# Optimization experiments

Hardware: AMD Instinct MI355X
Metric: run time of the kernel (lower is better)

Reference implementation:

```python
import jax, jax.numpy as jnp
import numpy as np

N_NODES = 100000


def setup_inputs() -> dict:
    key = jax.random.key(0)
    k1, k2, k3, k4 = jax.random.split(key, 4)
    E = 1600000
    D_IN, D_OUT = 128, 128
    feat = jax.random.normal(k1, (N_NODES, D_IN), dtype=jnp.float32)
    src = jax.random.randint(k2, (E,), 0, N_NODES, dtype=jnp.int32)
    dst = jax.random.randint(k3, (E,), 0, N_NODES, dtype=jnp.int32)
    # xavier_uniform for weight [in, out]
    limit = float(np.sqrt(6.0 / (D_IN + D_OUT)))
    weight = jax.random.uniform(k4, (D_IN, D_OUT), dtype=jnp.float32,
                                minval=-limit, maxval=limit)
    bias = jnp.zeros((D_OUT,), dtype=jnp.float32)
    return {"feat": feat, "weight": weight, "bias": bias, "src": src, "dst": dst}


def reference(feat, weight, bias, src, dst):
    # in-degree normalization: norm_i = 1/sqrt(in_deg(i)); clamp deg>=1 to avoid inf
    deg = jax.ops.segment_sum(jnp.ones(src.shape[0], dtype=jnp.float32), dst,
                              num_segments=N_NODES)
    norm = jax.lax.rsqrt(jnp.maximum(deg, 1.0))[:, None]  # [N,1]
    h = feat * norm
    # update_all(copy_src, sum): scatter-sum src features into dst nodes (SpMM)
    agg = jax.ops.segment_sum(h[src], dst, num_segments=N_NODES)  # [N, D_in]
    # in_feats == out_feats -> aggregate first, then dense transform
    rst = agg @ weight          # [N, D_out]
    rst = rst * norm + bias
    return rst
```

## Files before the change

### kernel.cpp

```cpp
#include <hip/hip_runtime.h>


constexpr int N_NODES = 100000;
constexpr int D = 128;
constexpr int NB = 256;
constexpr int GROUP = (N_NODES + NB - 1) / NB;
constexpr int CAP = 14336;
constexpr int CONVB = 1280;
constexpr int RPAD = 136;

typedef float f32x4 __attribute__((ext_vector_type(4)));
typedef short short8 __attribute__((ext_vector_type(8)));
typedef unsigned uint4v __attribute__((ext_vector_type(4)));

__device__ __forceinline__ ushort f2bf(float x) {
    unsigned u = __float_as_uint(x);
    return (ushort)((u + 0x7fffu + ((u >> 16) & 1u)) >> 16);
}
__device__ __forceinline__ float bf2f(ushort h) {
    return __uint_as_float(((unsigned)h) << 16);
}

__global__ __launch_bounds__(256) void p1_histo_conv(const int* __restrict__ dst, int E,
                                                     int* __restrict__ bhist,
                                                     const float* __restrict__ W,
                                                     ushort* __restrict__ whi,
                                                     ushort* __restrict__ wlo,
                                                     const float* __restrict__ feat,
                                                     uint2* __restrict__ ft2) {
    int t = threadIdx.x, blk = blockIdx.x;
    if (blk >= NB) {
        int base = (blk - NB) * 256 + t;
        int stride = CONVB * 256;
        for (int i = base; i < N_NODES * 32; i += stride) {
            f32x4 v = ((const f32x4*)feat)[i];
            uint2 o;
            o.x = (unsigned)f2bf(v[0]) | ((unsigned)f2bf(v[1]) << 16);
            o.y = (unsigned)f2bf(v[2]) | ((unsigned)f2bf(v[3]) << 16);
            ft2[i] = o;
        }
        return;
    }
    __shared__ int h[NB];
    h[t] = 0;
    if (blk < 64) {
        int p = blk * 256 + t;
        int i  = p & 7;
        int l  = (p >> 3) & 63;
        int kt = (p >> 9) & 3;
        int ct = (p >> 11);
        int k = kt * 32 + (l >> 4) * 8 + i;
        int n = ct * 16 + (l & 15);
        float x = W[k * 128 + n];
        ushort hh = f2bf(x);
        whi[p] = hh;
        wlo[p] = f2bf(x - bf2f(hh));
    }
    __syncthreads();
    int per = (E + NB - 1) / NB;
    int s = blk * per, e = min(E, s + per);
    for (int i = s + t; i < e; i += 256) atomicAdd(&h[dst[i] / GROUP], 1);
    __syncthreads();
    bhist[t * NB + blk] = h[t];
}

__global__ __launch_bounds__(256) void p1_scanrow(int* __restrict__ bhist,
                                                  int* __restrict__ rowtot) {
    __shared__ int lds[256];
    int b = blockIdx.x, t = threadIdx.x;
    int v = bhist[b * NB + t];
    lds[t] = v; __syncthreads();
    for (int off = 1; off < 256; off <<= 1) {
        int x = (t >= off) ? lds[t - off] : 0;
        __syncthreads();
        lds[t] += x;
        __syncthreads();
    }
    bhist[b * NB + t] = lds[t] - v;
    if (t == 255) rowtot[b] = lds[255];
}

__global__ __launch_bounds__(256) void p1_scatter(const int* __restrict__ src,
                                                  const int* __restrict__ dst, int E,
                                                  const int* __restrict__ bhist,
                                                  const int* __restrict__ rowtot,
                                                  int* __restrict__ pairs) {
    __shared__ int loff[NB];
    __shared__ int bb[NB];
    int t = threadIdx.x, blk = blockIdx.x;
    int rv = rowtot[t];
    bb[t] = rv; __syncthreads();
    for (int off = 1; off < 256; off <<= 1) {
        int x = (t >= off) ? bb[t - off] : 0;
        __syncthreads();
        bb[t] += x;
        __syncthreads();
    }
    loff[t] = bhist[t * NB + blk] + bb[t] - rv;
    __syncthreads();
    int per = (E + NB - 1) / NB;
    int s = blk * per, e = min(E, s + per);
    for (int i = s + t; i < e; i += 256) {
        int d = dst[i];
        int b = d / GROUP;
        int pos = atomicAdd(&loff[b], 1);
        pairs[pos] = ((d - b * GROUP) << 17) | src[i];
    }
}

__global__ __launch_bounds__(256) void p2_all(const int* __restrict__ pairs,
                                              const int* __restrict__ rowtot,
                                              int* __restrict__ deg,
                                              int* __restrict__ offs,
                                              float* __restrict__ norm,
                                              int* __restrict__ esrc) {
    __shared__ int h[512];
    __shared__ int ssum[256];
    __shared__ int bb[256];
    __shared__ int sbuf[CAP];
    int t = threadIdx.x, b = blockIdx.x;
    int lo = b * GROUP;
    int cnt = min(GROUP, N_NODES - lo);

    int rv = rowtot[t];
    bb[t] = rv;
    h[t] = 0; h[t + 256] = 0;
    __syncthreads();
    for (int off = 1; off < 256; off <<= 1) {
        int x = (t >= off) ? bb[t - off] : 0;
        __syncthreads();
        bb[t] += x;
        __syncthreads();
    }
    int s1 = bb[b];
    int s0 = s1 - rowtot[b];
    __syncthreads();

    for (int i = s0 + t; i < s1; i += 256) atomicAdd(&h[pairs[i] >> 17], 1);
    __syncthreads();

    int v0 = h[2 * t], v1 = h[2 * t + 1];
    int s = v0 + v1;
    ssum[t] = s; __syncthreads();
    for (int off = 1; off < 256; off <<= 1) {
        int x = (t >= off) ? ssum[t - off] : 0;
        __syncthreads();
        ssum[t] += x;
        __syncthreads();
    }
    int pre = ssum[t] - s;
    if (2 * t < cnt) {
        int node = lo + 2 * t;
        deg[node] = v0;
        offs[node] = s0 + pre;
        norm[node] = rsqrtf(fmaxf((float)v0, 1.0f));
    }
    if (2 * t + 1 < cnt) {
        int node = lo + 2 * t + 1;
        deg[node] = v1;
        offs[node] = s0 + pre + v0;
        norm[node] = rsqrtf(fmaxf((float)v1, 1.0f));
    }
    __syncthreads();
    h[2 * t] = pre;
    h[2 * t + 1] = pre + v0;
    __syncthreads();

    int wsize = s1 - s0;
    bool fits = (wsize <= CAP);
    for (int i = s0 + t; i < s1; i += 256) {
        int p = pairs[i];
        int dl = p >> 17;
        int sv = p & 0x1FFFF;
        int pos = atomicAdd(&h[dl], 1);
        if (fits) sbuf[pos] = sv; else esrc[s0 + pos] = sv;
    }
    __syncthreads();
    if (fits)
        for (int i = t; i < wsize; i += 256) esrc[s0 + i] = sbuf[i];
}

__global__ __launch_bounds__(256) void k_gather_gemm(const unsigned* __restrict__ ft,
                                                     const int* __restrict__ offs,
                                                     const int* __restrict__ deg,
                                                     const int* __restrict__ esrc,
                                                     const float* __restrict__ norm,
                                                     const ushort* __restrict__ whi,
                                                     const ushort* __restrict__ wlo,
                                                     const float* __restrict__ bias,
                                                     float* __restrict__ out) {
    __shared__ ushort sA[16 * RPAD];
    const int wid  = threadIdx.x >> 6;
    const int lane = threadIdx.x & 63;
    const int g  = lane >> 4;
    const int sl = lane & 15;
    const int row0 = blockIdx.x * 16;
    const uint4v* ftv = (const uint4v*)ft;

    #pragma unroll
    for (int n4 = 0; n4 < 4; ++n4) {
        int n = wid * 4 + n4;
        int node = row0 + n;
        int start = offs[node];
        int cnt   = deg[node];
        int last  = start + cnt - 1;
        float acc[8] = {0.f, 0.f, 0.f, 0.f, 0.f, 0.f, 0.f, 0.f};
        for (int j = 0; j < cnt; j += 16) {
            int i0 = start + j + g;
            int s0v = esrc[min(i0,      last)];
            int s1v = esrc[min(i0 + 4,  last)];
            int s2v = esrc[min(i0 + 8,  last)];
            int s3v = esrc[min(i0 + 12, last)];
            float w0 = (j + g      < cnt) ? norm[s0v] : 0.0f;
            float w1 = (j + g + 4  < cnt) ? norm[s1v] : 0.0f;
            float w2 = (j + g + 8  < cnt) ? norm[s2v] : 0.0f;
            float w3 = (j + g + 12 < cnt) ? norm[s3v] : 0.0f;
            uint4v u0 = ftv[(size_t)s0v * 16 + sl];
            uint4v u1 = ftv[(size_t)s1v * 16 + sl];
            uint4v u2 = ftv[(size_t)s2v * 16 + sl];
            uint4v u3 = ftv[(size_t)s3v * 16 + sl];
            #pragma unroll
            for (int q = 0; q < 4; ++q) {
                unsigned a = u0[q];
                acc[q * 2]     = fmaf(__uint_as_float(a << 16),         w0, acc[q * 2]);
                acc[q * 2 + 1] = fmaf(__uint_as_float(a & 0xffff0000u), w0, acc[q * 2 + 1]);
            }
            #pragma unroll
            for (int q = 0; q < 4; ++q) {
                unsigned a = u1[q];
                acc[q * 2]     = fmaf(__uint_as_float(a << 16),         w1, acc[q * 2]);
                acc[q * 2 + 1] = fmaf(__uint_as_float(a & 0xffff0000u), w1, acc[q * 2 + 1]);
            }
            #pragma unroll
            for (int q = 0; q < 4; ++q) {
                unsigned a = u2[q];
                acc[q * 2]     = fmaf(__uint_as_float(a << 16),         w2, acc[q * 2]);
                acc[q * 2 + 1] = fmaf(__uint_as_float(a & 0xffff0000u), w2, acc[q * 2 + 1]);
            }
            #pragma unroll
            for (int q = 0; q < 4; ++q) {
                unsigned a = u3[q];
                acc[q * 2]     = fmaf(__uint_as_float(a << 16),         w3, acc[q * 2]);
                acc[q * 2 + 1] = fmaf(__uint_as_float(a & 0xffff0000u), w3, acc[q * 2 + 1]);
            }
        }
        #pragma unroll
        for (int q = 0; q < 8; ++q) {
            acc[q] += __shfl_xor(acc[q], 16, 64);
            acc[q] += __shfl_xor(acc[q], 32, 64);
        }
        if (g == 0) {
            uint4v o;
            #pragma unroll
            for (int q = 0; q < 4; ++q)
                o[q] = (unsigned)f2bf(acc[q * 2]) | ((unsigned)f2bf(acc[q * 2 + 1]) << 16);
            *(uint4v*)(&sA[n * RPAD + sl * 8]) = o;
        }
    }
    __syncthreads();

    const int rsub = lane & 15;
    const int kgrp = lane >> 4;
    short8 a[4];
    #pragma unroll
    for (int kt = 0; kt < 4; ++kt)
        a[kt] = *(const short8*)(&sA[rsub * RPAD + kt * 32 + kgrp * 8]);
    float nr[4];
    #pragma unroll
    for (int r = 0; r < 4; ++r) nr[r] = norm[row0 + kgrp * 4 + r];

    const short8* BH = (const short8*)whi;
    const short8* BL = (const short8*)wlo;
    #pragma unroll
    for (int cc = 0; cc < 2; ++cc) {
        int ct = wid * 2 + cc;
        f32x4 acc = {0.f, 0.f, 0.f, 0.f};
        #pragma unroll
        for (int kt = 0; kt < 4; ++kt) {
            acc = __builtin_amdgcn_mfma_f32_16x16x32_bf16(a[kt], BH[(ct * 4 + kt) * 64 + lane], acc, 0, 0, 0);
            acc = __builtin_amdgcn_mfma_f32_16x16x32_bf16(a[kt], BL[(ct * 4 + kt) * 64 + lane], acc, 0, 0, 0);
        }
        const float bc = bias[ct * 16 + rsub];
        float* ocol = out + (size_t)row0 * D + ct * 16 + rsub;
        #pragma unroll
        for (int r = 0; r < 4; ++r) {
            int row = kgrp * 4 + r;
            ocol[(size_t)row * D] = acc[r] * nr[r] + bc;
        }
    }
}

__global__ void k_scatter(const float* __restrict__ feat, const int* __restrict__ src,
                          const int* __restrict__ dst, const float* __restrict__ norm,
                          int E, float* __restrict__ agg) {
    long long gtid = (long long)blockIdx.x * blockDim.x + threadIdx.x;
    int e    = (int)(gtid >> 6);
    int lane = (int)(gtid & 63);
    if (e >= E) return;
    int s = src[e];
    int t = dst[e];
    float ns = norm[s];
    float2 v = ((const float2*)(feat + (size_t)s * D))[lane];
    float* arow = agg + (size_t)t * D + lane * 2;
    atomicAdd(arow + 0, v.x * ns);
    atomicAdd(arow + 1, v.y * ns);
}
__global__ void k_deg_f(const int* __restrict__ dst, int E, float* __restrict__ deg) {
    int i = blockIdx.x * blockDim.x + threadIdx.x;
    if (i < E) atomicAdd(deg + dst[i], 1.0f);
}
__global__ void k_norm_f(float* __restrict__ dn) {
    int i = blockIdx.x * blockDim.x + threadIdx.x;
    if (i < N_NODES) dn[i] = rsqrtf(fmaxf(dn[i], 1.0f));
}
__global__ __launch_bounds__(256) void k_gemm(float* __restrict__ io,
                                              const float* __restrict__ W,
                                              const float* __restrict__ bias,
                                              const float* __restrict__ norm) {
    __shared__ float sW[D * D];
    __shared__ float srow[2][D];
    for (int i = threadIdx.x; i < D * D; i += 256) sW[i] = W[i];
    const int r = threadIdx.x >> 7;
    const int c = threadIdx.x & 127;
    const float bc = bias[c];
    const int npairs = N_NODES / 2;
    for (int rp = blockIdx.x; rp < npairs; rp += gridDim.x) {
        __syncthreads();
        const int row = rp * 2 + r;
        srow[r][c] = io[(size_t)row * D + c];
        __syncthreads();
        float acc = 0.f;
        #pragma unroll 8
        for (int k = 0; k < D; ++k)
            acc = fmaf(srow[r][k], sW[k * D + c], acc);
        io[(size_t)row * D + c] = acc * norm[row] + bc;
    }
}

extern "C" void kernel_launch(void* const* d_in, const int* in_sizes, int n_in,
                              void* d_out, int out_size, void* d_ws, size_t ws_size,
                              hipStream_t stream) {
    const float* feat   = (const float*)d_in[0];
    const float* weight = (const float*)d_in[1];
    const float* bias   = (const float*)d_in[2];
    const int*   src    = (const int*)d_in[3];
    const int*   dst    = (const int*)d_in[4];
    const int E = in_sizes[3];

    int* pairs = (int*)d_out;

    uintptr_t cur = (uintptr_t)d_ws;
    auto take = [&](size_t bytes) -> void* {
        uintptr_t r = (cur + 63) & ~(uintptr_t)63;
        cur = r + bytes;
        return (void*)r;
    };

    size_t S_ft  = (size_t)N_NODES * 64 * 4;
    size_t need  = S_ft +
                   (size_t)(3 * N_NODES + 256 + NB * NB + E) * 4 + 65536 + 1024;

    unsigned* ft     = (unsigned*)take(S_ft);
    float*    norm   = (float*)take((size_t)N_NODES * 4);
    int*      deg    = (int*)take((size_t)N_NODES * 4);
    int*      offs   = (int*)take((size_t)N_NODES * 4);
    int*      rowtot = (int*)take(256 * 4);
    int*      bhist  = (int*)take((size_t)NB * NB * 4);
    int*      esrc   = (int*)take((size_t)E * 4);
    ushort*   whi    = (ushort*)take(16384 * 2);
    ushort*   wlo    = (ushort*)take(16384 * 2);

    if (ws_size >= need) {
        p1_histo_conv<<<NB + CONVB, 256, 0, stream>>>(dst, E, bhist, weight, whi, wlo,
                                                      feat, (uint2*)ft);
        p1_scanrow<<<NB, 256, 0, stream>>>(bhist, rowtot);
        p1_scatter<<<NB, 256, 0, stream>>>(src, dst, E, bhist, rowtot, pairs);
        p2_all<<<NB, 256, 0, stream>>>(pairs, rowtot, deg, offs, norm, esrc);
        k_gather_gemm<<<N_NODES / 16, 256, 0, stream>>>(ft, offs, deg, esrc, norm,
                                                        whi, wlo, bias, (float*)d_out);
    } else {
        float* agg = (float*)d_out;
        hipMemsetAsync(d_out, 0, (size_t)N_NODES * D * sizeof(float), stream);
        hipMemsetAsync(norm, 0, (size_t)N_NODES * sizeof(float), stream);
        k_deg_f<<<(E + 255) / 256, 256, 0, stream>>>(dst, E, (float*)norm);
        k_norm_f<<<(N_NODES + 255) / 256, 256, 0, stream>>>((float*)norm);
        long long sthreads = (long long)E * 64;
        k_scatter<<<(int)((sthreads + 255) / 256), 256, 0, stream>>>(feat, src, dst, (float*)norm, E, agg);
        k_gemm<<<4096, 256, 0, stream>>>(agg, weight, bias, (float*)norm);
    }
}
```

Measured before the change: 133.7 us.

## Fuse sort preprocessing kernels into one cooperative kernel with grid syncs

Replaces the four launches (histogram/convert, row scan, scatter, per-bucket sort) with a single cooperative kernel that uses grid.sync between phases. The bf16 feature conversion now runs on the same 256 blocks with an 8-way unrolled loop, instead of on 1280 extra blocks. This removes launch gaps and inter-kernel drains. It risks lower parallelism for the conversion and the cost of the grid barriers, and it falls back to the old path if the cooperative launch fails.

New measurement: 236.8 us. 77.2% more time.

```diff
diff --git a/kernel.cpp b/kernel.cpp
--- a/kernel.cpp
+++ b/kernel.cpp
@@ -1,4 +1,7 @@
 #include <hip/hip_runtime.h>
+#include <hip/hip_cooperative_groups.h>
+
+namespace cg = cooperative_groups;
 
 
 constexpr int N_NODES = 100000;
@@ -19,6 +22,181 @@
 }
 __device__ __forceinline__ float bf2f(ushort h) {
     return __uint_as_float(((unsigned)h) << 16);
+}
+__device__ __forceinline__ uint2 conv4(const f32x4 v) {
+    uint2 o;
+    o.x = (unsigned)f2bf(v[0]) | ((unsigned)f2bf(v[1]) << 16);
+    o.y = (unsigned)f2bf(v[2]) | ((unsigned)f2bf(v[3]) << 16);
+    return o;
+}
+
+__global__ __launch_bounds__(256) void k_sort_coop(const int* __restrict__ src,
+                                                   const int* __restrict__ dst, int E,
+                                                   const float* __restrict__ W,
+                                                   ushort* __restrict__ whi,
+                                                   ushort* __restrict__ wlo,
+                                                   const float* __restrict__ feat,
+                                                   uint2* __restrict__ ft2,
+                                                   int* __restrict__ bhist,
+                                                   int* __restrict__ rowtot,
+                                                   int* __restrict__ pairs,
+                                                   int* __restrict__ deg,
+                                                   int* __restrict__ offs,
+                                                   float* __restrict__ norm,
+                                                   int* __restrict__ esrc) {
+    cg::grid_group grid = cg::this_grid();
+    __shared__ int sh_h[512];
+    __shared__ int sh_a[256];
+    __shared__ int sh_b[256];
+    __shared__ int sbuf[CAP];
+    const int t = threadIdx.x, b = blockIdx.x;
+
+    if (b < 64) {
+        int p = b * 256 + t;
+        int i  = p & 7;
+        int l  = (p >> 3) & 63;
+        int kt = (p >> 9) & 3;
+        int ct = (p >> 11);
+        int k = kt * 32 + (l >> 4) * 8 + i;
+        int n = ct * 16 + (l & 15);
+        float x = W[k * 128 + n];
+        ushort hh = f2bf(x);
+        whi[p] = hh;
+        wlo[p] = f2bf(x - bf2f(hh));
+    }
+
+    {
+        const int total = N_NODES * 32;
+        const int stride = NB * 256;
+        int i = b * 256 + t;
+        const f32x4* fv = (const f32x4*)feat;
+        for (; i + 7 * stride < total; i += 8 * stride) {
+            f32x4 v0 = fv[i];
+            f32x4 v1 = fv[i + stride];
+            f32x4 v2 = fv[i + 2 * stride];
+            f32x4 v3 = fv[i + 3 * stride];
+            f32x4 v4 = fv[i + 4 * stride];
+            f32x4 v5 = fv[i + 5 * stride];
+            f32x4 v6 = fv[i + 6 * stride];
+            f32x4 v7 = fv[i + 7 * stride];
+            ft2[i]              = conv4(v0);
+            ft2[i + stride]     = conv4(v1);
+            ft2[i + 2 * stride] = conv4(v2);
+            ft2[i + 3 * stride] = conv4(v3);
+            ft2[i + 4 * stride] = conv4(v4);
+            ft2[i + 5 * stride] = conv4(v5);
+            ft2[i + 6 * stride] = conv4(v6);
+            ft2[i + 7 * stride] = conv4(v7);
+        }
+        for (; i < total; i += stride) ft2[i] = conv4(((const f32x4*)feat)[i]);
+    }
+
+    sh_h[t] = 0;
+    __syncthreads();
+    const int per = (E + NB - 1) / NB;
+    {
+        int s = b * per, e = min(E, s + per);
+        for (int i = s + t; i < e; i += 256) atomicAdd(&sh_h[dst[i] / GROUP], 1);
+    }
+    __syncthreads();
+    bhist[t * NB + b] = sh_h[t];
+    grid.sync();
+
+    {
+        int v = bhist[b * NB + t];
+        sh_a[t] = v; __syncthreads();
+        for (int off = 1; off < 256; off <<= 1) {
+            int x = (t >= off) ? sh_a[t - off] : 0;
+            __syncthreads();
+            sh_a[t] += x;
+            __syncthreads();
+        }
+        bhist[b * NB + t] = sh_a[t] - v;
+        if (t == 255) rowtot[b] = sh_a[255];
+    }
+    grid.sync();
+
+    {
+        int rv = rowtot[t];
+        sh_a[t] = rv; __syncthreads();
+        for (int off = 1; off < 256; off <<= 1) {
+            int x = (t >= off) ? sh_a[t - off] : 0;
+            __syncthreads();
+            sh_a[t] += x;
+            __syncthreads();
+        }
+        sh_b[t] = bhist[t * NB + b] + sh_a[t] - rv;
+        __syncthreads();
+        int s = b * per, e = min(E, s + per);
+        for (int i = s + t; i < e; i += 256) {
+            int d = dst[i];
+            int bk = d / GROUP;
+            int pos = atomicAdd(&sh_b[bk], 1);
+            pairs[pos] = ((d - bk * GROUP) << 17) | src[i];
+        }
+    }
+    grid.sync();
+
+    {
+        int lo = b * GROUP;
+        int cnt = min(GROUP, N_NODES - lo);
+        int rv = rowtot[t];
+        sh_a[t] = rv;
+        sh_h[t] = 0; sh_h[t + 256] = 0;
+        __syncthreads();
+        for (int off = 1; off < 256; off <<= 1) {
+            int x = (t >= off) ? sh_a[t - off] : 0;
+            __syncthreads();
+            sh_a[t] += x;
+            __syncthreads();
+        }
+        int s1 = sh_a[b];
+        int s0 = s1 - rowtot[b];
+        __syncthreads();
+
+        for (int i = s0 + t; i < s1; i += 256) atomicAdd(&sh_h[pairs[i] >> 17], 1);
+        __syncthreads();
+
+        int v0 = sh_h[2 * t], v1 = sh_h[2 * t + 1];
+        int s = v0 + v1;
+        sh_b[t] = s; __syncthreads();
+        for (int off = 1; off < 256; off <<= 1) {
+            int x = (t >= off) ? sh_b[t - off] : 0;
+            __syncthreads();
+            sh_b[t] += x;
+            __syncthreads();
+        }
+        int pre = sh_b[t] - s;
+        if (2 * t < cnt) {
+            int node = lo + 2 * t;
+            deg[node] = v0;
+            offs[node] = s0 + pre;
+            norm[node] = rsqrtf(fmaxf((float)v0, 1.0f));
+        }
+        if (2 * t + 1 < cnt) {
+            int node = lo + 2 * t + 1;
+            deg[node] = v1;
+            offs[node] = s0 + pre + v0;
+            norm[node] = rsqrtf(fmaxf((float)v1, 1.0f));
+        }
+        __syncthreads();
+        sh_h[2 * t] = pre;
+        sh_h[2 * t + 1] = pre + v0;
+        __syncthreads();
+
+        int wsize = s1 - s0;
+        bool fits = (wsize <= CAP);
+        for (int i = s0 + t; i < s1; i += 256) {
+            int p = pairs[i];
+            int dl = p >> 17;
+            int sv = p & 0x1FFFF;
+            int pos = atomicAdd(&sh_h[dl], 1);
+            if (fits) sbuf[pos] = sv; else esrc[s0 + pos] = sv;
+        }
+        __syncthreads();
+        if (fits)
+            for (int i = t; i < wsize; i += 256) esrc[s0 + i] = sbuf[i];
+    }
 }
 
 __global__ __launch_bounds__(256) void p1_histo_conv(const int* __restrict__ dst, int E,
@@ -32,13 +210,8 @@
     if (blk >= NB) {
         int base = (blk - NB) * 256 + t;
         int stride = CONVB * 256;
-        for (int i = base; i < N_NODES * 32; i += stride) {
-            f32x4 v = ((const f32x4*)feat)[i];
-            uint2 o;
-            o.x = (unsigned)f2bf(v[0]) | ((unsigned)f2bf(v[1]) << 16);
-            o.y = (unsigned)f2bf(v[2]) | ((unsigned)f2bf(v[3]) << 16);
-            ft2[i] = o;
-        }
+        for (int i = base; i < N_NODES * 32; i += stride)
+            ft2[i] = conv4(((const f32x4*)feat)[i]);
         return;
     }
     __shared__ int h[NB];
@@ -345,7 +518,7 @@
     const float* bias   = (const float*)d_in[2];
     const int*   src    = (const int*)d_in[3];
     const int*   dst    = (const int*)d_in[4];
-    const int E = in_sizes[3];
+    int E = in_sizes[3];
 
     int* pairs = (int*)d_out;
 
@@ -371,11 +544,20 @@
     ushort*   wlo    = (ushort*)take(16384 * 2);
 
     if (ws_size >= need) {
-        p1_histo_conv<<<NB + CONVB, 256, 0, stream>>>(dst, E, bhist, weight, whi, wlo,
-                                                      feat, (uint2*)ft);
-        p1_scanrow<<<NB, 256, 0, stream>>>(bhist, rowtot);
-        p1_scatter<<<NB, 256, 0, stream>>>(src, dst, E, bhist, rowtot, pairs);
-        p2_all<<<NB, 256, 0, stream>>>(pairs, rowtot, deg, offs, norm, esrc);
+        uint2* ft2 = (uint2*)ft;
+        void* args[] = {(void*)&src, (void*)&dst, (void*)&E, (void*)&weight,
+                        (void*)&whi, (void*)&wlo, (void*)&feat, (void*)&ft2,
+                        (void*)&bhist, (void*)&rowtot, (void*)&pairs,
+                        (void*)&deg, (void*)&offs, (void*)&norm, (void*)&esrc};
+        hipError_t err = hipLaunchCooperativeKernel((const void*)k_sort_coop,
+                                                    dim3(NB), dim3(256), args, 0, stream);
+        if (err != hipSuccess) {
+            p1_histo_conv<<<NB + CONVB, 256, 0, stream>>>(dst, E, bhist, weight, whi, wlo,
+                                                          feat, (uint2*)ft);
+            p1_scanrow<<<NB, 256, 0, stream>>>(bhist, rowtot);
+            p1_scatter<<<NB, 256, 0, stream>>>(src, dst, E, bhist, rowtot, pairs);
+            p2_all<<<NB, 256, 0, stream>>>(pairs, rowtot, deg, offs, norm, esrc);
+        }
         k_gather_gemm<<<N_NODES / 16, 256, 0, stream>>>(ft, offs, deg, esrc, norm,
                                                         whi, wlo, bias, (float*)d_out);
     } else {
```
